# Performance work log

Hardware: AMD Instinct MI355X
Metric: run time of the kernel (lower is better)

## Reference

```python
import jax, jax.numpy as jnp
import numpy as np


def setup_inputs() -> dict:
    key = jax.random.key(0)
    k1, k2, k3, k4, k5 = jax.random.split(key, 5)
    V, E = 512, 256  # num_nodes, num_edges
    l_v = jax.random.normal(k1, (V,), dtype=jnp.float32)
    h = jax.random.randint(k2, (E, V), 0, 2, dtype=jnp.int32)  # binary parity-check matrix
    s_c = jax.random.randint(k3, (E,), 0, 2).astype(jnp.float32)  # syndrome bits in {0,1}
    b = jax.random.uniform(k4, (V,), dtype=jnp.float32)
    w = jax.random.uniform(k5, (V, E), dtype=jnp.float32)
    return {"l_v": l_v, "h": h, "s_c": s_c, "b": b, "w": w, "iterations": 5}


def reference(l_v, h, s_c, b, w, iterations):
    V = l_v.shape[0]
    E = s_c.shape[0]
    hT = h.T                                   # [V, E] entries (used as indices, values in {0,1})
    v_idx = jnp.arange(V)[:, None]             # [V, 1]
    c_idx = jnp.arange(E)[:, None]             # [E, 1]
    sign_c = (1.0 - 2.0 * s_c)[:, None]        # (-1)**s_c for s in {0,1}
    base = (l_v * b)[:, None]                  # [V, 1]

    mu_vc = jnp.zeros((V, E), dtype=jnp.float32)  # v -> c messages
    mu_cv = jnp.zeros((E, V), dtype=jnp.float32)  # c -> v messages

    for _ in range(int(iterations)):
        # ---- v -> c: message[v,c] = tanh(0.5*(l_v[v]*b[v] + sum_{e: h[e,v]!=c} mu_cv[h[e,v],v]*w[v,h[e,v]]))
        contrib = mu_cv[hT, v_idx] * w[v_idx, hT]          # [V, E]: term for each row e of h
        total = contrib.sum(axis=1, keepdims=True)          # [V, 1]
        # subtract terms where the index value h[e,v] equals the target check c (scatter-add)
        sub = jnp.zeros((V, E), dtype=jnp.float32).at[v_idx, hT].add(contrib)  # [V, E]
        mu_vc_new = jnp.tanh(0.5 * (base + total - sub))    # [V, E]

        # ---- c -> v: message[c,v] = (-1)**s_c * 2*atanh(prod_{j: h[c,j]!=v} tanh(mu_vc[h[c,j],c]/2))
        tvals = jnp.tanh(0.5 * mu_vc[h, c_idx])             # [E, V] per-entry tanh terms
        # mask out entries whose value equals target v, then product over j
        masked = jnp.where(h[:, None, :] == jnp.arange(V)[None, :, None],
                           jnp.float32(1.0), tvals[:, None, :])  # [E, V, V]
        prod = masked.prod(axis=2)                          # [E, V]
        mu_cv_new = sign_c * 2.0 * jnp.arctanh(prod)        # [E, V]

        mu_vc, mu_cv = mu_vc_new, mu_cv_new

    # ---- marginalization (no exclusion)
    contrib = mu_cv[hT, v_idx] * w[v_idx, hT]               # [V, E]
    mu_v = jnp.tanh(0.5 * (l_v * b + contrib.sum(axis=1)))  # [V]
    return 1.0 / (jnp.exp(mu_v) + 1.0)
```

## Files before the change

kernel.cpp:

```cpp
#include <hip/hip_runtime.h>
#include <math.h>


#define V_N 512
#define E_N 256

__device__ inline float ipowf_(float x, int n) {
    float r = 1.0f, p = x;
    while (n > 0) {
        if (n & 1) r *= p;
        p *= p;
        n >>= 1;
    }
    return r;
}

__global__ __launch_bounds__(1024) void bp_kernel(
    const float* __restrict__ l_v, const int* __restrict__ h,
    const float* __restrict__ s_c, const float* __restrict__ b,
    const float* __restrict__ w, const int* __restrict__ it_p,
    float* __restrict__ out)
{
    const int t = threadIdx.x;
    const int v = t & (V_N - 1);
    const int half = t >> 9;

    __shared__ int cntsh[1024];
    __shared__ int red0[V_N], red1[V_N];
    __shared__ float csh[8];

    int part = 0;
    const int ebase = half * (E_N / 2);
    #pragma unroll 8
    for (int e = 0; e < E_N / 2; ++e) {
        part += h[(ebase + e) * V_N + v];
    }
    cntsh[t] = part;

    if (half == 0) {
        red0[v] = h[v];
        red1[v] = h[V_N + v];
    }
    __syncthreads();
    for (int off = V_N / 2; off > 0; off >>= 1) {
        if (t < off) { red0[t] += red0[t + off]; red1[t] += red1[t + off]; }
        __syncthreads();
    }

    if (t == 0) {
        const int iters = it_p[0];
        const int n1_0 = red0[0], n1_1 = red1[0];
        const int n0_0 = V_N - n1_0, n0_1 = V_N - n1_1;
        const int cnt1_0 = cntsh[0] + cntsh[V_N + 0];
        const int cnt1_1 = cntsh[1] + cntsh[V_N + 1];
        const int cnt0_0 = E_N - cnt1_0, cnt0_1 = E_N - cnt1_1;
        const float base0 = l_v[0] * b[0];
        const float base1 = l_v[1] * b[1];
        const float w00 = w[0],     w01 = w[1];
        const float w10 = w[E_N],   w11 = w[E_N + 1];
        const float sg0 = 1.0f - 2.0f * s_c[0];
        const float sg1 = 1.0f - 2.0f * s_c[1];

        float V0c0 = 0.f, V0c1 = 0.f;
        float V1c0 = 0.f, V1c1 = 0.f;
        float C0v0 = 0.f, C0v1 = 0.f, C0vR = 0.f;
        float C1v0 = 0.f, C1v1 = 0.f, C1vR = 0.f;

        for (int it = 0; it < iters; ++it) {
            float T0 = (float)cnt0_0 * C0v0 * w00;
            float T1 = (float)cnt1_0 * C1v0 * w01;
            float tot = T0 + T1;
            float nV0c0 = tanhf(0.5f * (base0 + tot - T0));
            float nV0c1 = tanhf(0.5f * (base0 + tot - T1));
            T0 = (float)cnt0_1 * C0v1 * w10;
            T1 = (float)cnt1_1 * C1v1 * w11;
            tot = T0 + T1;
            float nV1c0 = tanhf(0.5f * (base1 + tot - T0));
            float nV1c1 = tanhf(0.5f * (base1 + tot - T1));

            float t0 = tanhf(0.5f * V0c0);
            float t1 = tanhf(0.5f * V1c0);
            float p0 = ipowf_(t0, n0_0);
            float p1 = ipowf_(t1, n1_0);
            float nC0v0 = sg0 * 2.0f * atanhf(p1);
            float nC0v1 = sg0 * 2.0f * atanhf(p0);
            float nC0vR = sg0 * 2.0f * atanhf(p0 * p1);
            t0 = tanhf(0.5f * V0c1);
            t1 = tanhf(0.5f * V1c1);
            p0 = ipowf_(t0, n0_1);
            p1 = ipowf_(t1, n1_1);
            float nC1v0 = sg1 * 2.0f * atanhf(p1);
            float nC1v1 = sg1 * 2.0f * atanhf(p0);
            float nC1vR = sg1 * 2.0f * atanhf(p0 * p1);

            V0c0 = nV0c0; V0c1 = nV0c1;
            V1c0 = nV1c0; V1c1 = nV1c1;
            C0v0 = nC0v0; C0v1 = nC0v1; C0vR = nC0vR;
            C1v0 = nC1v0; C1v1 = nC1v1; C1vR = nC1vR;
        }
        csh[0] = C0v0; csh[1] = C0v1; csh[2] = C0vR;
        csh[3] = C1v0; csh[4] = C1v1; csh[5] = C1vR;
    }
    __syncthreads();

    if (half == 0) {
        const int cnt1 = cntsh[v] + cntsh[V_N + v];
        const int cnt0 = E_N - cnt1;
        const float basev = l_v[v] * b[v];
        const float wv0 = w[v * E_N + 0];
        const float wv1 = w[v * E_N + 1];
        const float c0 = (v == 0) ? csh[0] : (v == 1) ? csh[1] : csh[2];
        const float c1 = (v == 0) ? csh[3] : (v == 1) ? csh[4] : csh[5];
        const float s = basev + (float)cnt0 * c0 * wv0 + (float)cnt1 * c1 * wv1;
        const float mu = tanhf(0.5f * s);
        out[v] = 1.0f / (expf(mu) + 1.0f);
    }
}

extern "C" void kernel_launch(void* const* d_in, const int* in_sizes, int n_in,
                              void* d_out, int out_size, void* d_ws, size_t ws_size,
                              hipStream_t stream) {
    const float* l_v   = (const float*)d_in[0];
    const int*   h     = (const int*)  d_in[1];
    const float* s_c   = (const float*)d_in[2];
    const float* b     = (const float*)d_in[3];
    const float* w     = (const float*)d_in[4];
    const int*   iters = (const int*)  d_in[5];
    float* out = (float*)d_out;
    hipLaunchKernelGGL(bp_kernel, dim3(1), dim3(1024), 0, stream,
                       l_v, h, s_c, b, w, iters, out);
}
```

Measured before the change: 23.77 us.

## Split column-count reduction into multi-block pre-kernel and use wave shuffles

Moves the per-column popcount over all 256 rows of h out of the single-block kernel into a 32-block kernel using int4 loads, writing partial sums to workspace. The solve kernel then sums 16 partials per thread instead of 128 rows. The tree reductions over the first two rows of h become wavefront shuffle reductions, and the tot-minus-T algebra is simplified. This adds a second kernel launch and a workspace round trip in exchange for spreading the memory-bound reduction across many CUs.

```diff
diff --git a/kernel.cpp b/kernel.cpp
--- a/kernel.cpp
+++ b/kernel.cpp
@@ -4,6 +4,7 @@
 
 #define V_N 512
 #define E_N 256
+#define BLK1 32
 
 __device__ inline float ipowf_(float x, int n) {
     float r = 1.0f, p = x;
@@ -15,41 +16,64 @@
     return r;
 }
 
-__global__ __launch_bounds__(1024) void bp_kernel(
+__global__ __launch_bounds__(256) void bp_count(const int* __restrict__ h,
+                                                int* __restrict__ ws) {
+    const int b = blockIdx.x, t = threadIdx.x;
+    const int cg = t & 127;
+    const int rh = t >> 7;
+    const int4* h4 = (const int4*)h;
+    const int rowbase = b * 8 + rh * 4;
+    int4 acc = make_int4(0, 0, 0, 0);
+    #pragma unroll
+    for (int r = 0; r < 4; ++r) {
+        int4 x = h4[(rowbase + r) * (V_N / 4) + cg];
+        acc.x += x.x; acc.y += x.y; acc.z += x.z; acc.w += x.w;
+    }
+    __shared__ int4 p[2][128];
+    p[rh][cg] = acc;
+    __syncthreads();
+    if (t < 128) {
+        int4 a = p[0][t], c = p[1][t];
+        ((int4*)ws)[b * 128 + t] =
+            make_int4(a.x + c.x, a.y + c.y, a.z + c.z, a.w + c.w);
+    }
+}
+
+__global__ __launch_bounds__(1024) void bp_solve(
     const float* __restrict__ l_v, const int* __restrict__ h,
     const float* __restrict__ s_c, const float* __restrict__ b,
     const float* __restrict__ w, const int* __restrict__ it_p,
-    float* __restrict__ out)
+    const int* __restrict__ ws, float* __restrict__ out)
 {
     const int t = threadIdx.x;
     const int v = t & (V_N - 1);
     const int half = t >> 9;
 
     __shared__ int cntsh[1024];
-    __shared__ int red0[V_N], red1[V_N];
+    __shared__ int wred[16][2];
     __shared__ float csh[8];
 
     int part = 0;
-    const int ebase = half * (E_N / 2);
-    #pragma unroll 8
-    for (int e = 0; e < E_N / 2; ++e) {
-        part += h[(ebase + e) * V_N + v];
-    }
+    #pragma unroll
+    for (int bb = 0; bb < BLK1 / 2; ++bb)
+        part += ws[(half * (BLK1 / 2) + bb) * V_N + v];
     cntsh[t] = part;
 
-    if (half == 0) {
-        red0[v] = h[v];
-        red1[v] = h[V_N + v];
+    int r0 = 0, r1 = 0;
+    if (half == 0) { r0 = h[v]; r1 = h[V_N + v]; }
+    #pragma unroll
+    for (int off = 32; off > 0; off >>= 1) {
+        r0 += __shfl_down(r0, off);
+        r1 += __shfl_down(r1, off);
     }
+    if ((t & 63) == 0) { wred[t >> 6][0] = r0; wred[t >> 6][1] = r1; }
     __syncthreads();
-    for (int off = V_N / 2; off > 0; off >>= 1) {
-        if (t < off) { red0[t] += red0[t + off]; red1[t] += red1[t + off]; }
-        __syncthreads();
-    }
 
     if (t == 0) {
+        int n1_0 = 0, n1_1 = 0;
+        #pragma unroll
+        for (int wv = 0; wv < 8; ++wv) { n1_0 += wred[wv][0]; n1_1 += wred[wv][1]; }
         const int iters = it_p[0];
-        const int n1_0 = red0[0], n1_1 = red1[0];
         const int n0_0 = V_N - n1_0, n0_1 = V_N - n1_1;
         const int cnt1_0 = cntsh[0] + cntsh[V_N + 0];
         const int cnt1_1 = cntsh[1] + cntsh[V_N + 1];
@@ -61,22 +85,19 @@
         const float sg0 = 1.0f - 2.0f * s_c[0];
         const float sg1 = 1.0f - 2.0f * s_c[1];
 
-        float V0c0 = 0.f, V0c1 = 0.f;
-        float V1c0 = 0.f, V1c1 = 0.f;
+        float V0c0 = 0.f, V0c1 = 0.f, V1c0 = 0.f, V1c1 = 0.f;
         float C0v0 = 0.f, C0v1 = 0.f, C0vR = 0.f;
         float C1v0 = 0.f, C1v1 = 0.f, C1vR = 0.f;
 
         for (int it = 0; it < iters; ++it) {
             float T0 = (float)cnt0_0 * C0v0 * w00;
             float T1 = (float)cnt1_0 * C1v0 * w01;
-            float tot = T0 + T1;
-            float nV0c0 = tanhf(0.5f * (base0 + tot - T0));
-            float nV0c1 = tanhf(0.5f * (base0 + tot - T1));
+            float nV0c0 = tanhf(0.5f * (base0 + T1));
+            float nV0c1 = tanhf(0.5f * (base0 + T0));
             T0 = (float)cnt0_1 * C0v1 * w10;
             T1 = (float)cnt1_1 * C1v1 * w11;
-            tot = T0 + T1;
-            float nV1c0 = tanhf(0.5f * (base1 + tot - T0));
-            float nV1c1 = tanhf(0.5f * (base1 + tot - T1));
+            float nV1c0 = tanhf(0.5f * (base1 + T1));
+            float nV1c1 = tanhf(0.5f * (base1 + T0));
 
             float t0 = tanhf(0.5f * V0c0);
             float t1 = tanhf(0.5f * V1c0);
@@ -93,8 +114,7 @@
             float nC1v1 = sg1 * 2.0f * atanhf(p0);
             float nC1vR = sg1 * 2.0f * atanhf(p0 * p1);
 
-            V0c0 = nV0c0; V0c1 = nV0c1;
-            V1c0 = nV1c0; V1c1 = nV1c1;
+            V0c0 = nV0c0; V0c1 = nV0c1; V1c0 = nV1c0; V1c1 = nV1c1;
             C0v0 = nC0v0; C0v1 = nC0v1; C0vR = nC0vR;
             C1v0 = nC1v0; C1v1 = nC1v1; C1vR = nC1vR;
         }
@@ -127,6 +147,9 @@
     const float* w     = (const float*)d_in[4];
     const int*   iters = (const int*)  d_in[5];
     float* out = (float*)d_out;
-    hipLaunchKernelGGL(bp_kernel, dim3(1), dim3(1024), 0, stream,
-                       l_v, h, s_c, b, w, iters, out);
+    int*   ws  = (int*)d_ws;
+
+    hipLaunchKernelGGL(bp_count, dim3(BLK1), dim3(256), 0, stream, h, ws);
+    hipLaunchKernelGGL(bp_solve, dim3(1), dim3(1024), 0, stream,
+                       l_v, h, s_c, b, w, iters, ws, out);
 }
```

Result: slower. 24.27 us (+2.1%).
